# Performance work log

Hardware: AMD Instinct MI355X
Metric: run time of the kernel (lower is better)

The kernel has to match this reference:

```python
import jax, jax.numpy as jnp
import numpy as np
from jax import lax

ALPHA = 0.99
D_MODEL = 2048


def setup_inputs() -> dict:
    key = jax.random.key(0)
    x = jax.random.normal(key, (4, 4096, D_MODEL), dtype=jnp.float32)
    return {"x": x}


def reference(x) -> jnp.ndarray:
    # EMA recurrence: ema_t = alpha * ema_{t-1} + (1 - alpha) * x_t, ema_{-1} = 0
    b, s, d = x.shape
    alpha = jnp.asarray(ALPHA, dtype=x.dtype)
    one_m = jnp.asarray(1.0 - ALPHA, dtype=x.dtype)

    def step(ema, xt):  # ema: [b, d], xt: [b, d]
        ema = alpha * ema + one_m * xt
        return ema, ema

    ema0 = jnp.zeros((b, d), dtype=x.dtype)
    _, ys = lax.scan(step, ema0, jnp.swapaxes(x, 0, 1))  # ys: [s, b, d]
    return jnp.swapaxes(ys, 0, 1)  # [b, s, d]
```

## Files before the change

### kernel.cpp

```cpp
#include <hip/hip_runtime.h>


namespace {

constexpr int B  = 4;
constexpr int S  = 4096;
constexpr int D  = 2048;
constexpr int D4 = D / 4;
constexpr int NCOL4 = B * D4;
constexpr int BLOCK = 256;

typedef float v4f __attribute__((ext_vector_type(4)));

constexpr float kA  = 0.99f;
constexpr float kOm = (float)(1.0 - 0.99);

constexpr double alpha_pow_pow2(int l) {
    double t = 0.99;
    while (l > 1) { t *= t; l >>= 1; }
    return t;
}

template <int NCHUNK>
__global__ __launch_bounds__(BLOCK)
void cema_k1_finals(const float4* __restrict__ x, float4* __restrict__ ws) {
    constexpr int L = S / NCHUNK;
    const int c  = blockIdx.x * BLOCK + threadIdx.x;
    const int j  = blockIdx.y;
    const int b  = c >> 9;
    const int d4 = c & (D4 - 1);

    const size_t base = ((size_t)b * S + (size_t)j * L) * D4 + d4;
    const float4* p = x + base;

    float e0 = 0.f, e1 = 0.f, e2 = 0.f, e3 = 0.f;
#pragma unroll 8
    for (int t = 0; t < L; ++t) {
        float4 v = p[(size_t)t * D4];
        e0 = kA * e0 + kOm * v.x;
        e1 = kA * e1 + kOm * v.y;
        e2 = kA * e2 + kOm * v.z;
        e3 = kA * e3 + kOm * v.w;
    }
    ws[(size_t)j * NCOL4 + c] = make_float4(e0, e1, e2, e3);
}

template <int NCHUNK>
__global__ __launch_bounds__(BLOCK)
void cema_k2_apply(const float4* __restrict__ x, const float4* __restrict__ ws,
                   float4* __restrict__ out) {
    constexpr int L = S / NCHUNK;
    constexpr float aL = (float)alpha_pow_pow2(L);

    const int c  = blockIdx.x * BLOCK + threadIdx.x;
    const int j  = blockIdx.y;
    const int b  = c >> 9;
    const int d4 = c & (D4 - 1);

    float E0 = 0.f, E1 = 0.f, E2 = 0.f, E3 = 0.f;
#pragma unroll 4
    for (int i = 0; i < j; ++i) {
        float4 f = ws[(size_t)i * NCOL4 + c];
        E0 = E0 * aL + f.x;
        E1 = E1 * aL + f.y;
        E2 = E2 * aL + f.z;
        E3 = E3 * aL + f.w;
    }

    const size_t base = ((size_t)b * S + (size_t)j * L) * D4 + d4;
    const float4* p = x + base;
    v4f* q = (v4f*)(out + base);

#pragma unroll 8
    for (int t = 0; t < L; ++t) {
        float4 v = p[(size_t)t * D4];
        E0 = kA * E0 + kOm * v.x;
        E1 = kA * E1 + kOm * v.y;
        E2 = kA * E2 + kOm * v.z;
        E3 = kA * E3 + kOm * v.w;
        v4f o = {E0, E1, E2, E3};
        __builtin_nontemporal_store(o, &q[(size_t)t * D4]);
    }
}

template <int NCHUNK>
void launch(const float4* x, float4* ws, float4* out, hipStream_t stream) {
    dim3 grid(NCOL4 / BLOCK, NCHUNK);
    cema_k1_finals<NCHUNK><<<grid, BLOCK, 0, stream>>>(x, ws);
    cema_k2_apply<NCHUNK><<<grid, BLOCK, 0, stream>>>(x, ws, out);
}

}

extern "C" void kernel_launch(void* const* d_in, const int* in_sizes, int n_in,
                              void* d_out, int out_size, void* d_ws, size_t ws_size,
                              hipStream_t stream) {
    const float4* x  = (const float4*)d_in[0];
    float4* out      = (float4*)d_out;
    float4* ws       = (float4*)d_ws;

    const size_t per_chunk = (size_t)NCOL4 * sizeof(float4);
    if (ws_size >= 128 * per_chunk)      launch<128>(x, ws, out, stream);
    else if (ws_size >= 64 * per_chunk)  launch<64>(x, ws, out, stream);
    else                                 launch<32>(x, ws, out, stream);
}
```

Measured before the change: 253.2 us.

## Fuse chunk-final and apply passes into one kernel with inter-block flags

Merges the two EMA kernels into a single kernel. Each block first computes its chunk's final EMA partial and publishes it with a release-flag. It then spin-waits with acquire loads until all earlier chunks in its column group have published, folds their partials, and applies the recurrence to write the output. A small kernel zeroes the flags beforehand. The intent is to remove the second kernel launch and the global barrier between passes, and to re-read each x chunk while it is likely still cached. The cost is spin-wait synchronization that relies on all blocks being co-resident, plus extra workspace for the flags.

```diff
diff --git a/kernel.cpp b/kernel.cpp
--- a/kernel.cpp
+++ b/kernel.cpp
@@ -9,6 +9,7 @@
 constexpr int D4 = D / 4;
 constexpr int NCOL4 = B * D4;
 constexpr int BLOCK = 256;
+constexpr int XB = NCOL4 / BLOCK;
 
 typedef float v4f __attribute__((ext_vector_type(4)));
 
@@ -21,11 +22,21 @@
     return t;
 }
 
+__global__ __launch_bounds__(256)
+void zero_flags(int* __restrict__ flags, int n) {
+    int i = blockIdx.x * 256 + threadIdx.x;
+    if (i < n) flags[i] = 0;
+}
+
 template <int NCHUNK>
-__global__ __launch_bounds__(BLOCK)
-void cema_k1_finals(const float4* __restrict__ x, float4* __restrict__ ws) {
+__global__ __launch_bounds__(BLOCK, 4)
+void cema_fused(const float4* __restrict__ x, float4* __restrict__ out,
+                float4* __restrict__ part, int* __restrict__ flags) {
     constexpr int L = S / NCHUNK;
-    const int c  = blockIdx.x * BLOCK + threadIdx.x;
+    constexpr float aL = (float)alpha_pow_pow2(L);
+
+    const int xb = blockIdx.x;
+    const int c  = xb * BLOCK + threadIdx.x;
     const int j  = blockIdx.y;
     const int b  = c >> 9;
     const int d4 = c & (D4 - 1);
@@ -33,44 +44,48 @@
     const size_t base = ((size_t)b * S + (size_t)j * L) * D4 + d4;
     const float4* p = x + base;
 
-    float e0 = 0.f, e1 = 0.f, e2 = 0.f, e3 = 0.f;
+    float f0 = 0.f, f1 = 0.f, f2 = 0.f, f3 = 0.f;
 #pragma unroll 8
     for (int t = 0; t < L; ++t) {
         float4 v = p[(size_t)t * D4];
-        e0 = kA * e0 + kOm * v.x;
-        e1 = kA * e1 + kOm * v.y;
-        e2 = kA * e2 + kOm * v.z;
-        e3 = kA * e3 + kOm * v.w;
+        f0 = kA * f0 + kOm * v.x;
+        f1 = kA * f1 + kOm * v.y;
+        f2 = kA * f2 + kOm * v.z;
+        f3 = kA * f3 + kOm * v.w;
     }
-    ws[(size_t)j * NCOL4 + c] = make_float4(e0, e1, e2, e3);
-}
 
-template <int NCHUNK>
-__global__ __launch_bounds__(BLOCK)
-void cema_k2_apply(const float4* __restrict__ x, const float4* __restrict__ ws,
-                   float4* __restrict__ out) {
-    constexpr int L = S / NCHUNK;
-    constexpr float aL = (float)alpha_pow_pow2(L);
-
-    const int c  = blockIdx.x * BLOCK + threadIdx.x;
-    const int j  = blockIdx.y;
-    const int b  = c >> 9;
-    const int d4 = c & (D4 - 1);
+    part[(size_t)j * NCOL4 + c] = make_float4(f0, f1, f2, f3);
+    __threadfence();
+    __syncthreads();
+    if (threadIdx.x == 0)
+        __hip_atomic_store(&flags[xb * NCHUNK + j], 1,
+                           __ATOMIC_RELEASE, __HIP_MEMORY_SCOPE_AGENT);
 
     float E0 = 0.f, E1 = 0.f, E2 = 0.f, E3 = 0.f;
+    if (j > 0) {
+        const int t = threadIdx.x;
+        for (;;) {
+            int ok = 1;
+            if (t < j)
+                ok = (__hip_atomic_load(&flags[xb * NCHUNK + t],
+                                        __ATOMIC_ACQUIRE, __HIP_MEMORY_SCOPE_AGENT) != 0);
+            if (__syncthreads_and(ok)) break;
+            __builtin_amdgcn_s_sleep(2);
+        }
+        __threadfence();
+
+        const float4* w = part + c;
 #pragma unroll 4
-    for (int i = 0; i < j; ++i) {
-        float4 f = ws[(size_t)i * NCOL4 + c];
-        E0 = E0 * aL + f.x;
-        E1 = E1 * aL + f.y;
-        E2 = E2 * aL + f.z;
-        E3 = E3 * aL + f.w;
+        for (int i = 0; i < j; ++i) {
+            float4 f = w[(size_t)i * NCOL4];
+            E0 = E0 * aL + f.x;
+            E1 = E1 * aL + f.y;
+            E2 = E2 * aL + f.z;
+            E3 = E3 * aL + f.w;
+        }
     }
 
-    const size_t base = ((size_t)b * S + (size_t)j * L) * D4 + d4;
-    const float4* p = x + base;
     v4f* q = (v4f*)(out + base);
-
 #pragma unroll 8
     for (int t = 0; t < L; ++t) {
         float4 v = p[(size_t)t * D4];
@@ -84,10 +99,11 @@
 }
 
 template <int NCHUNK>
-void launch(const float4* x, float4* ws, float4* out, hipStream_t stream) {
-    dim3 grid(NCOL4 / BLOCK, NCHUNK);
-    cema_k1_finals<NCHUNK><<<grid, BLOCK, 0, stream>>>(x, ws);
-    cema_k2_apply<NCHUNK><<<grid, BLOCK, 0, stream>>>(x, ws, out);
+void launch(const float4* x, float4* out, float4* ws, hipStream_t stream) {
+    int* flags = (int*)(ws + (size_t)NCHUNK * NCOL4);
+    const int nflags = XB * NCHUNK;
+    zero_flags<<<dim3((nflags + 255) / 256), dim3(256), 0, stream>>>(flags, nflags);
+    cema_fused<NCHUNK><<<dim3(XB, NCHUNK), dim3(BLOCK), 0, stream>>>(x, out, ws, flags);
 }
 
 }
@@ -95,12 +111,14 @@
 extern "C" void kernel_launch(void* const* d_in, const int* in_sizes, int n_in,
                               void* d_out, int out_size, void* d_ws, size_t ws_size,
                               hipStream_t stream) {
-    const float4* x  = (const float4*)d_in[0];
-    float4* out      = (float4*)d_out;
-    float4* ws       = (float4*)d_ws;
+    const float4* x = (const float4*)d_in[0];
+    float4* out     = (float4*)d_out;
+    float4* ws      = (float4*)d_ws;
 
-    const size_t per_chunk = (size_t)NCOL4 * sizeof(float4);
-    if (ws_size >= 128 * per_chunk)      launch<128>(x, ws, out, stream);
-    else if (ws_size >= 64 * per_chunk)  launch<64>(x, ws, out, stream);
-    else                                 launch<32>(x, ws, out, stream);
+    auto need = [](size_t nchunk) {
+        return nchunk * NCOL4 * sizeof(float4) + (size_t)XB * nchunk * sizeof(int);
+    };
+    if (ws_size >= need(128))      launch<128>(x, out, ws, stream);
+    else if (ws_size >= need(64))  launch<64>(x, out, ws, stream);
+    else                           launch<32>(x, out, ws, stream);
 }
```

New measurement: 604.4 us. 139% more time.

## Add separate carry-scan kernel over chunk finals instead of per-chunk prefix loop

Applied to the files above, without the earlier changes.

Chunk-final states are now scanned once per column in a dedicated middle kernel that writes an exclusive carry per chunk. The apply kernel then reads a single carry value instead of looping over all earlier chunk finals. This removes the quadratic, imbalanced prefix work in the apply stage. In exchange it adds a third launch with a serial loop over chunks, and it needs twice the workspace, which may push the chunk count down to 64 or 32.

```diff
diff --git a/kernel.cpp b/kernel.cpp
--- a/kernel.cpp
+++ b/kernel.cpp
@@ -8,6 +8,7 @@
 constexpr int D  = 2048;
 constexpr int D4 = D / 4;
 constexpr int NCOL4 = B * D4;
+constexpr int NCOLS = NCOL4 * 4;
 constexpr int BLOCK = 256;
 
 typedef float v4f __attribute__((ext_vector_type(4)));
@@ -23,7 +24,7 @@
 
 template <int NCHUNK>
 __global__ __launch_bounds__(BLOCK)
-void cema_k1_finals(const float4* __restrict__ x, float4* __restrict__ ws) {
+void cema_k1_finals(const float4* __restrict__ x, float4* __restrict__ finals) {
     constexpr int L = S / NCHUNK;
     const int c  = blockIdx.x * BLOCK + threadIdx.x;
     const int j  = blockIdx.y;
@@ -42,30 +43,38 @@
         e2 = kA * e2 + kOm * v.z;
         e3 = kA * e3 + kOm * v.w;
     }
-    ws[(size_t)j * NCOL4 + c] = make_float4(e0, e1, e2, e3);
+    finals[(size_t)j * NCOL4 + c] = make_float4(e0, e1, e2, e3);
 }
 
 template <int NCHUNK>
 __global__ __launch_bounds__(BLOCK)
-void cema_k2_apply(const float4* __restrict__ x, const float4* __restrict__ ws,
+void cema_scan_finals(const float* __restrict__ finals, float* __restrict__ carry) {
+    constexpr int L = S / NCHUNK;
+    constexpr float aL = (float)alpha_pow_pow2(L);
+
+    const int col = blockIdx.x * BLOCK + threadIdx.x;
+    float E = 0.f;
+#pragma unroll 8
+    for (int j = 0; j < NCHUNK; ++j) {
+        float f = finals[(size_t)j * NCOLS + col];
+        carry[(size_t)j * NCOLS + col] = E;
+        E = E * aL + f;
+    }
+}
+
+template <int NCHUNK>
+__global__ __launch_bounds__(BLOCK)
+void cema_k3_apply(const float4* __restrict__ x, const float4* __restrict__ carry,
                    float4* __restrict__ out) {
     constexpr int L = S / NCHUNK;
-    constexpr float aL = (float)alpha_pow_pow2(L);
 
     const int c  = blockIdx.x * BLOCK + threadIdx.x;
     const int j  = blockIdx.y;
     const int b  = c >> 9;
     const int d4 = c & (D4 - 1);
 
-    float E0 = 0.f, E1 = 0.f, E2 = 0.f, E3 = 0.f;
-#pragma unroll 4
-    for (int i = 0; i < j; ++i) {
-        float4 f = ws[(size_t)i * NCOL4 + c];
-        E0 = E0 * aL + f.x;
-        E1 = E1 * aL + f.y;
-        E2 = E2 * aL + f.z;
-        E3 = E3 * aL + f.w;
-    }
+    float4 E4 = carry[(size_t)j * NCOL4 + c];
+    float E0 = E4.x, E1 = E4.y, E2 = E4.z, E3 = E4.w;
 
     const size_t base = ((size_t)b * S + (size_t)j * L) * D4 + d4;
     const float4* p = x + base;
@@ -85,9 +94,14 @@
 
 template <int NCHUNK>
 void launch(const float4* x, float4* ws, float4* out, hipStream_t stream) {
+    float4* finals = ws;
+    float4* carry  = ws + (size_t)NCHUNK * NCOL4;
+
     dim3 grid(NCOL4 / BLOCK, NCHUNK);
-    cema_k1_finals<NCHUNK><<<grid, BLOCK, 0, stream>>>(x, ws);
-    cema_k2_apply<NCHUNK><<<grid, BLOCK, 0, stream>>>(x, ws, out);
+    cema_k1_finals<NCHUNK><<<grid, BLOCK, 0, stream>>>(x, finals);
+    cema_scan_finals<NCHUNK><<<dim3(NCOLS / BLOCK), BLOCK, 0, stream>>>(
+        (const float*)finals, (float*)carry);
+    cema_k3_apply<NCHUNK><<<grid, BLOCK, 0, stream>>>(x, carry, out);
 }
 
 }
@@ -99,8 +113,10 @@
     float4* out      = (float4*)d_out;
     float4* ws       = (float4*)d_ws;
 
-    const size_t per_chunk = (size_t)NCOL4 * sizeof(float4);
-    if (ws_size >= 128 * per_chunk)      launch<128>(x, ws, out, stream);
-    else if (ws_size >= 64 * per_chunk)  launch<64>(x, ws, out, stream);
-    else                                 launch<32>(x, ws, out, stream);
+    auto need = [](size_t nchunk) {
+        return 2 * nchunk * (size_t)NCOL4 * sizeof(float4);
+    };
+    if (ws_size >= need(128))      launch<128>(x, ws, out, stream);
+    else if (ws_size >= need(64))  launch<64>(x, ws, out, stream);
+    else                           launch<32>(x, ws, out, stream);
 }
```

Result: slower. 261.1 us (+3.1%).

## Fuse chunk-final and apply passes into one cooperative kernel with grid sync

Applied to the files above, without the earlier changes.

Replaces the two-kernel chunked scan with a single cooperative kernel. Each block computes its chunk's final EMA state, writes it to the workspace, does a grid-wide sync, then combines earlier chunk finals and writes its output chunk. This removes the second kernel launch and the boundary between the two passes, and keeps every block resident. In exchange it needs the whole grid to be co-resident, at 4 blocks per CU, and it pays for a grid barrier. If the cooperative launch fails, it falls back to the original two kernels.

```diff
diff --git a/kernel.cpp b/kernel.cpp
--- a/kernel.cpp
+++ b/kernel.cpp
@@ -1,5 +1,8 @@
 #include <hip/hip_runtime.h>
+#include <hip/hip_cooperative_groups.h>
 
+
+namespace cg = cooperative_groups;
 
 namespace {
 
@@ -9,6 +12,7 @@
 constexpr int D4 = D / 4;
 constexpr int NCOL4 = B * D4;
 constexpr int BLOCK = 256;
+constexpr int XB = NCOL4 / BLOCK;
 
 typedef float v4f __attribute__((ext_vector_type(4)));
 
@@ -20,6 +24,62 @@
     while (l > 1) { t *= t; l >>= 1; }
     return t;
 }
+
+
+template <int NCHUNK>
+__global__ __launch_bounds__(BLOCK, 4)
+void cema_coop(const float4* __restrict__ x, float4* __restrict__ finals,
+               float4* __restrict__ out) {
+    constexpr int L = S / NCHUNK;
+    constexpr float aL = (float)alpha_pow_pow2(L);
+
+    const int xb = blockIdx.x;
+    const int c  = xb * BLOCK + threadIdx.x;
+    const int j  = blockIdx.y;
+    const int b  = c >> 9;
+    const int d4 = c & (D4 - 1);
+
+    const size_t base = ((size_t)b * S + (size_t)j * L) * D4 + d4;
+    const float4* p = x + base;
+
+    float f0 = 0.f, f1 = 0.f, f2 = 0.f, f3 = 0.f;
+#pragma unroll 8
+    for (int t = 0; t < L; ++t) {
+        float4 v = p[(size_t)t * D4];
+        f0 = kA * f0 + kOm * v.x;
+        f1 = kA * f1 + kOm * v.y;
+        f2 = kA * f2 + kOm * v.z;
+        f3 = kA * f3 + kOm * v.w;
+    }
+    finals[(size_t)j * NCOL4 + c] = make_float4(f0, f1, f2, f3);
+
+    __threadfence();
+    cg::this_grid().sync();
+
+    float E0 = 0.f, E1 = 0.f, E2 = 0.f, E3 = 0.f;
+    const float4* w = finals + c;
+#pragma unroll 4
+    for (int i = 0; i < j; ++i) {
+        float4 f = w[(size_t)i * NCOL4];
+        E0 = E0 * aL + f.x;
+        E1 = E1 * aL + f.y;
+        E2 = E2 * aL + f.z;
+        E3 = E3 * aL + f.w;
+    }
+
+    v4f* q = (v4f*)(out + base);
+#pragma unroll 8
+    for (int t = 0; t < L; ++t) {
+        float4 v = p[(size_t)t * D4];
+        E0 = kA * E0 + kOm * v.x;
+        E1 = kA * E1 + kOm * v.y;
+        E2 = kA * E2 + kOm * v.z;
+        E3 = kA * E3 + kOm * v.w;
+        v4f o = {E0, E1, E2, E3};
+        __builtin_nontemporal_store(o, &q[(size_t)t * D4]);
+    }
+}
+
 
 template <int NCHUNK>
 __global__ __launch_bounds__(BLOCK)
@@ -83,11 +143,22 @@
     }
 }
 
+
 template <int NCHUNK>
 void launch(const float4* x, float4* ws, float4* out, hipStream_t stream) {
-    dim3 grid(NCOL4 / BLOCK, NCHUNK);
-    cema_k1_finals<NCHUNK><<<grid, BLOCK, 0, stream>>>(x, ws);
-    cema_k2_apply<NCHUNK><<<grid, BLOCK, 0, stream>>>(x, ws, out);
+    const float4* xa = x;
+    float4* fa = ws;
+    float4* oa = out;
+    void* args[] = { (void*)&xa, (void*)&fa, (void*)&oa };
+    hipError_t err = hipLaunchCooperativeKernel(
+        (const void*)cema_coop<NCHUNK>, dim3(XB, NCHUNK), dim3(BLOCK),
+        args, 0, stream);
+    if (err != hipSuccess) {
+        (void)hipGetLastError();
+        dim3 grid(XB, NCHUNK);
+        cema_k1_finals<NCHUNK><<<grid, BLOCK, 0, stream>>>(x, ws);
+        cema_k2_apply<NCHUNK><<<grid, BLOCK, 0, stream>>>(x, ws, out);
+    }
 }
 
 }
@@ -99,8 +170,10 @@
     float4* out      = (float4*)d_out;
     float4* ws       = (float4*)d_ws;
 
-    const size_t per_chunk = (size_t)NCOL4 * sizeof(float4);
-    if (ws_size >= 128 * per_chunk)      launch<128>(x, ws, out, stream);
-    else if (ws_size >= 64 * per_chunk)  launch<64>(x, ws, out, stream);
-    else                                 launch<32>(x, ws, out, stream);
+    auto need = [](size_t nchunk) {
+        return nchunk * (size_t)NCOL4 * sizeof(float4);
+    };
+    if (ws_size >= need(128))      launch<128>(x, ws, out, stream);
+    else if (ws_size >= need(64))  launch<64>(x, ws, out, stream);
+    else                           launch<32>(x, ws, out, stream);
 }
```

New measurement: 506.3 us. 99.9% more time.
